# Performance work log

Hardware: AMD Instinct MI355X
Metric: run time of the kernel (lower is better)

## Reference

```python
import jax, jax.numpy as jnp
import numpy as np

N = 16384      # total nodes
E = 262144     # edges (avg degree 16)
HID = 1024     # hidden_dim
D = 768        # internal_dim
R = 6          # num_relations
B = 4          # num_bases
L = 2          # num_gnn_layers
BN_EPS = 1e-5
LN_EPS = 1e-5


def setup_inputs() -> dict:
    key = jax.random.key(0)
    ks = jax.random.split(key, 16)
    s = 0.02
    return {
        "h_text": jax.random.normal(ks[0], (N, HID), jnp.float32),
        "edge_index": jax.random.randint(ks[1], (2, E), 0, N, jnp.int32),
        "edge_type": jax.random.randint(ks[2], (E,), 0, R, jnp.int32),
        # input projection
        "w_in": jax.random.normal(ks[3], (HID, D), jnp.float32) * s,
        "b_in": jnp.zeros((D,), jnp.float32),
        # per-layer RGCN params (stacked over L layers)
        "basis": jax.random.normal(ks[4], (L, B, D, D), jnp.float32) * s,
        "comp": jax.random.normal(ks[5], (L, R, B), jnp.float32),
        "root": jax.random.normal(ks[6], (L, D, D), jnp.float32) * s,
        "conv_bias": jnp.zeros((L, D), jnp.float32),
        # per-layer BatchNorm affine params
        "bn_gamma": jnp.ones((L, D), jnp.float32),
        "bn_beta": jnp.zeros((L, D), jnp.float32),
        # output projection + LayerNorm
        "w_out": jax.random.normal(ks[7], (D, HID), jnp.float32) * s,
        "b_out": jnp.zeros((HID,), jnp.float32),
        "ln_gamma": jnp.ones((HID,), jnp.float32),
        "ln_beta": jnp.zeros((HID,), jnp.float32),
    }


def _rgcn_conv(x, src, dst, edge_type, basis, comp, root, bias):
    """PyG RGCNConv with basis decomposition, per-relation mean aggregation."""
    n = x.shape[0]
    # relation weights: W_r = sum_b comp[r,b] * basis[b]  -> [R, D, D]
    W = jnp.einsum('rb,bio->rio', comp, basis)
    # transform every node by every relation once: [R, N, D]
    h_all = jnp.einsum('ni,rio->rno', x, W)
    # per-(relation, target) in-degree for mean normalization
    counts = jnp.zeros((R, n), x.dtype).at[edge_type, dst].add(1.0)
    norm = 1.0 / counts[edge_type, dst]            # each indexed count >= 1
    msg = h_all[edge_type, src] * norm[:, None]    # [E, D] gathered messages
    agg = jax.ops.segment_sum(msg, dst, num_segments=n)
    return agg + x @ root + bias


def _batchnorm(x, gamma, beta):
    mean = jnp.mean(x, axis=0)
    var = jnp.var(x, axis=0)  # biased, as in torch BN training forward
    return gamma * (x - mean) * jax.lax.rsqrt(var + BN_EPS) + beta


def _layernorm(x, gamma, beta):
    mean = jnp.mean(x, axis=-1, keepdims=True)
    var = jnp.var(x, axis=-1, keepdims=True)
    return gamma * (x - mean) * jax.lax.rsqrt(var + LN_EPS) + beta


def reference(h_text, edge_index, edge_type, w_in, b_in, basis, comp, root,
              conv_bias, bn_gamma, bn_beta, w_out, b_out, ln_gamma, ln_beta):
    src, dst = edge_index[0], edge_index[1]
    x = jax.nn.relu(h_text @ w_in + b_in)
    for l in range(L):
        h_in = x
        x = _rgcn_conv(x, src, dst, edge_type, basis[l], comp[l], root[l], conv_bias[l])
        x = jax.nn.relu(x)
        x = x + h_in
        x = _batchnorm(x, bn_gamma[l], bn_beta[l])
    h_final = x @ w_out + b_out
    return _layernorm(h_final, ln_gamma, ln_beta)
```

## Files before the change

### kernel.cpp

```cpp
#include <hip/hip_runtime.h>
#include <hip/hip_bf16.h>

#define NN 16384
#define NE 262144
#define HIDD 1024
#define DD 768
#define RR 6
#define BB 4
#define LL 2
#define BN_EPS 1e-5f
#define LN_EPS 1e-5f

typedef __attribute__((ext_vector_type(8))) short bf16x8;
typedef __attribute__((ext_vector_type(4))) float f32x4;

__device__ __forceinline__ float b2f(unsigned short u) {
  union { unsigned int i; float f; } c;
  c.i = ((unsigned int)u) << 16;
  return c.f;
}
__device__ __forceinline__ unsigned short f2b(float f) {
  union { float f; unsigned int u; } c;
  c.f = f;
  unsigned int x = c.u;
  x += 0x7FFFu + ((x >> 16) & 1u);
  return (unsigned short)(x >> 16);
}

__device__ __forceinline__ void gll16(const unsigned short* g, unsigned short* l) {
  __builtin_amdgcn_global_load_lds(
      (const __attribute__((address_space(1))) unsigned int*)g,
      (__attribute__((address_space(3))) unsigned int*)l, 16, 0, 0);
}

__global__ void k_detect(const unsigned short* __restrict__ h, int* __restrict__ flag) {
  __shared__ int sh[256];
  int cnt = 0;
  for (int k = 0; k < 256; ++k) {
    ushort4 t = *(const ushort4*)&h[(size_t)(k * 256 + threadIdx.x) * 4];
    if ((t.x & 0x7F80) == 0x7F80) cnt++;
    if ((t.y & 0x7F80) == 0x7F80) cnt++;
    if ((t.z & 0x7F80) == 0x7F80) cnt++;
    if ((t.w & 0x7F80) == 0x7F80) cnt++;
  }
  sh[threadIdx.x] = cnt;
  __syncthreads();
  if (threadIdx.x == 0) {
    int t = 0;
    for (int i = 0; i < 256; ++i) t += sh[i];
    flag[0] = (t > 16) ? 1 : 0;
  }
}

template <int MODE>
__device__ __forceinline__ float load1t(const void* p, size_t i, int isf32) {
  if (MODE == 1 || (MODE == 0 && isf32)) return ((const float*)p)[i];
  return b2f(((const unsigned short*)p)[i]);
}

__global__ void k_cvt8(const void* s0, const void* s1, const void* s2, const void* s3,
                       const void* s4, const void* s5, const void* s6, const void* s7,
                       float* __restrict__ fpar, const int* __restrict__ flagp) {
  const int isf32 = flagp[0];
  const int seg = blockIdx.y;
  const int lens[8] = {768, 48, 1536, 1536, 1536, 1024, 1024, 1024};
  const int offs_[8] = {0, 768, 816, 2352, 3888, 5424, 6448, 7472};
  const void* srcs[8] = {s0, s1, s2, s3, s4, s5, s6, s7};
  int i = blockIdx.x * 256 + threadIdx.x;
  if (i < lens[seg]) fpar[offs_[seg] + i] = load1t<0>(srcs[seg], i, isf32);
}

__global__ void k_cvtb(const void* __restrict__ in, unsigned short* __restrict__ out,
                       int n, const int* __restrict__ flagp) {
  const int isf32 = flagp[0];
  int i = blockIdx.x * 256 + threadIdx.x;
  if (i < n) out[i] = f2b(load1t<0>(in, (size_t)i, isf32));
}

__global__ void k_fill(float* __restrict__ out, long n, float val) {
  long i = (long)blockIdx.x * 256 + threadIdx.x;
  if (i < n) out[i] = val;
}

__global__ __launch_bounds__(256) void k_transpose(const void* __restrict__ src,
                                                   long ioff,
                                                   unsigned short* __restrict__ dst,
                                                   int I, int J, int dstStride,
                                                   int dstOff,
                                                   const int* __restrict__ flagp) {
  const int isf32 = flagp[0];
  __shared__ unsigned short t[64][65];
  const int j0 = blockIdx.x * 64, i0 = blockIdx.y * 64;
  const int tx = threadIdx.x & 63, ty = threadIdx.x >> 6;
  for (int rr = ty; rr < 64; rr += 4)
    t[rr][tx] = f2b(load1t<0>(src, (size_t)ioff + (size_t)(i0 + rr) * J + j0 + tx, isf32));
  __syncthreads();
  for (int rr = ty; rr < 64; rr += 4)
    dst[(size_t)(j0 + rr) * dstStride + dstOff + i0 + tx] = t[tx][rr];
}

__global__ __launch_bounds__(256) void k_tbatch(const void* __restrict__ root, long roff,
                                                const void* __restrict__ basis, long boff,
                                                unsigned short* __restrict__ BT,
                                                const int* __restrict__ flagp) {
  const int isf32 = flagp[0];
  const int z = blockIdx.z;
  const void* src = (z == 0) ? root : basis;
  const long off = (z == 0) ? roff : boff + (long)(z - 1) * DD * DD;
  __shared__ unsigned short t[64][65];
  const int j0 = blockIdx.x * 64, i0 = blockIdx.y * 64;
  const int tx = threadIdx.x & 63, ty = threadIdx.x >> 6;
  for (int rr = ty; rr < 64; rr += 4)
    t[rr][tx] = f2b(load1t<0>(src, (size_t)off + (size_t)(i0 + rr) * DD + j0 + tx, isf32));
  __syncthreads();
  for (int rr = ty; rr < 64; rr += 4)
    BT[(size_t)(j0 + rr) * (5 * DD) + z * DD + i0 + tx] = t[tx][rr];
}

template <int BIAS, int RELU, int OUTB>
__global__ __launch_bounds__(256) void k_mgemm(const unsigned short* __restrict__ A,
                                               const unsigned short* __restrict__ Bt,
                                               const float* __restrict__ bias,
                                               void* __restrict__ C,
                                               int M, int Nn, int K) {
  __shared__ __align__(16) unsigned short Alds[128 * 32];
  __shared__ __align__(16) unsigned short Blds[128 * 32];
  const int tid = threadIdx.x;
  const int lane = tid & 63, w = tid >> 6;
  const int wm = w >> 1, wn = w & 1;
  const int fr = lane & 15, kg = lane >> 4;
  const int nwg = gridDim.x;
  int id = blockIdx.x;
  if ((nwg & 7) == 0) id = (id & 7) * (nwg >> 3) + (id >> 3);
  const int gx = Nn >> 7;
  const int m0 = (id / gx) * 128, n0 = (id % gx) * 128;

  const int srow = w * 16 + (lane >> 2);
  const int sslot = (lane & 3) ^ ((lane >> 3) & 3);
  const unsigned short* ga = A + (size_t)(m0 + srow) * K + sslot * 8;
  const unsigned short* ga2 = ga + (size_t)64 * K;
  const unsigned short* gb = Bt + (size_t)(n0 + srow) * K + sslot * 8;
  const unsigned short* gb2 = gb + (size_t)64 * K;
  unsigned short* la = Alds + w * 512;
  unsigned short* lb = Blds + w * 512;
  const int roff = fr * 32 + ((kg ^ ((fr >> 1) & 3)) * 8);

  f32x4 acc[4][4] = {};

  for (int k0 = 0; k0 < K; k0 += 32) {
    gll16(ga + k0, la);
    gll16(ga2 + k0, la + 2048);
    gll16(gb + k0, lb);
    gll16(gb2 + k0, lb + 2048);
    __syncthreads();
    bf16x8 af[4], bfr[4];
#pragma unroll
    for (int i = 0; i < 4; ++i) {
      af[i] = *(const bf16x8*)(Alds + (wm * 4 + i) * 512 + roff);
      bfr[i] = *(const bf16x8*)(Blds + (wn * 4 + i) * 512 + roff);
    }
#pragma unroll
    for (int i = 0; i < 4; ++i)
#pragma unroll
      for (int j = 0; j < 4; ++j)
        acc[i][j] = __builtin_amdgcn_mfma_f32_16x16x32_bf16(af[i], bfr[j],
                                                            acc[i][j], 0, 0, 0);
    __syncthreads();
  }

  const int orow = (lane >> 4) * 4;
#pragma unroll
  for (int i = 0; i < 4; ++i) {
#pragma unroll
    for (int j = 0; j < 4; ++j) {
      const int n = n0 + wn * 64 + j * 16 + fr;
      const float bv = BIAS ? bias[n] : 0.f;
#pragma unroll
      for (int rg = 0; rg < 4; ++rg) {
        const int m = m0 + wm * 64 + i * 16 + orow + rg;
        const size_t off = (size_t)m * Nn + n;
        float v = acc[i][j][rg] + bv;
        if (RELU) v = fmaxf(v, 0.f);
        if (OUTB) ((unsigned short*)C)[off] = f2b(v);
        else      ((float*)C)[off] = v;
      }
    }
  }
}

__global__ __launch_bounds__(256) void k_mgemm3(const unsigned short* __restrict__ x0,
                                                const unsigned short* __restrict__ Y01,
                                                const unsigned short* __restrict__ Y23,
                                                const unsigned short* __restrict__ BT,
                                                float* __restrict__ C) {
  __shared__ __align__(16) unsigned short Alds[128 * 32];
  __shared__ __align__(16) unsigned short Blds[128 * 32];
  const int tid = threadIdx.x;
  const int lane = tid & 63, w = tid >> 6;
  const int wm = w >> 1, wn = w & 1;
  const int fr = lane & 15, kg = lane >> 4;
  const int nwg = gridDim.x;
  int id = blockIdx.x;
  id = (id & 7) * (nwg >> 3) + (id >> 3);
  const int m0 = (id / 6) * 128, n0 = (id % 6) * 128;

  const int srow = w * 16 + (lane >> 2);
  const int sslot = (lane & 3) ^ ((lane >> 3) & 3);
  const unsigned short* gx = x0 + (size_t)(m0 + srow) * DD + sslot * 8;
  const unsigned short* gx2 = gx + (size_t)64 * DD;
  const unsigned short* gy = Y01 + (size_t)(m0 + srow) * 1536 + sslot * 8;
  const unsigned short* gy2 = gy + (size_t)64 * 1536;
  const unsigned short* gz = Y23 + (size_t)(m0 + srow) * 1536 + sslot * 8;
  const unsigned short* gz2 = gz + (size_t)64 * 1536;
  const unsigned short* gb = BT + (size_t)(n0 + srow) * 3840 + sslot * 8;
  const unsigned short* gb2 = gb + (size_t)64 * 3840;
  unsigned short* la = Alds + w * 512;
  unsigned short* lb = Blds + w * 512;
  const int roff = fr * 32 + ((kg ^ ((fr >> 1) & 3)) * 8);

  f32x4 acc[4][4] = {};

  for (int k0 = 0; k0 < 3840; k0 += 32) {
    const unsigned short *pa, *pa2;
    if (k0 < 768)       { pa = gx + k0;        pa2 = gx2 + k0; }
    else if (k0 < 2304) { pa = gy + k0 - 768;  pa2 = gy2 + k0 - 768; }
    else                { pa = gz + k0 - 2304; pa2 = gz2 + k0 - 2304; }
    gll16(pa, la);
    gll16(pa2, la + 2048);
    gll16(gb + k0, lb);
    gll16(gb2 + k0, lb + 2048);
    __syncthreads();
    bf16x8 af[4], bfr[4];
#pragma unroll
    for (int i = 0; i < 4; ++i) {
      af[i] = *(const bf16x8*)(Alds + (wm * 4 + i) * 512 + roff);
      bfr[i] = *(const bf16x8*)(Blds + (wn * 4 + i) * 512 + roff);
    }
#pragma unroll
    for (int i = 0; i < 4; ++i)
#pragma unroll
      for (int j = 0; j < 4; ++j)
        acc[i][j] = __builtin_amdgcn_mfma_f32_16x16x32_bf16(af[i], bfr[j],
                                                            acc[i][j], 0, 0, 0);
    __syncthreads();
  }

  const int orow = (lane >> 4) * 4;
#pragma unroll
  for (int i = 0; i < 4; ++i) {
#pragma unroll
    for (int j = 0; j < 4; ++j) {
      const int n = n0 + wn * 64 + j * 16 + fr;
#pragma unroll
      for (int rg = 0; rg < 4; ++rg) {
        const int m = m0 + wm * 64 + i * 16 + orow + rg;
        C[(size_t)m * DD + n] = acc[i][j][rg];
      }
    }
  }
}

__global__ void k_count(const int* __restrict__ et, const int* __restrict__ dst,
                        float* __restrict__ counts) {
  int e = blockIdx.x * 256 + threadIdx.x;
  if (e < NE) atomicAdd(&counts[(size_t)et[e] * NN + dst[e]], 1.0f);
}

__global__ void k_deg(const int* __restrict__ dst, int* __restrict__ deg) {
  int e = blockIdx.x * 256 + threadIdx.x;
  if (e < NE) atomicAdd(&deg[dst[e]], 1);
}

__global__ __launch_bounds__(256) void k_scan(const int* __restrict__ deg,
                                              int* __restrict__ offs,
                                              int* __restrict__ cursor) {
  __shared__ int part[256];
  const int base = threadIdx.x * 64;
  int s = 0;
  for (int i = 0; i < 64; ++i) s += deg[base + i];
  part[threadIdx.x] = s;
  __syncthreads();
  if (threadIdx.x == 0) {
    int run = 0;
    for (int i = 0; i < 256; ++i) { int t = part[i]; part[i] = run; run += t; }
  }
  __syncthreads();
  int run = part[threadIdx.x];
  for (int i = 0; i < 64; ++i) {
    offs[base + i] = run;
    cursor[base + i] = run;
    run += deg[base + i];
  }
  if (threadIdx.x == 255) offs[NN] = run;
}

__global__ void k_place(const int* __restrict__ src, const int* __restrict__ dst,
                        const int* __restrict__ et, int* __restrict__ cursor,
                        int* __restrict__ elist) {
  int e = blockIdx.x * 256 + threadIdx.x;
  if (e >= NE) return;
  int d = dst[e];
  int slot = atomicAdd(&cursor[d], 1);
  elist[slot] = src[e] | (et[e] << 20);
}

__global__ __launch_bounds__(192) void k_gather4(const int* __restrict__ offs,
                                                 const int* __restrict__ elist,
                                                 const float* __restrict__ counts,
                                                 const float* __restrict__ compL,
                                                 const unsigned short* __restrict__ x0,
                                                 unsigned short* __restrict__ Y01,
                                                 unsigned short* __restrict__ Y23) {
  const int d = blockIdx.x;
  const int tid = threadIdx.x;
  __shared__ float sw[RR][4];
  if (tid < 4 * RR) {
    const int r = tid >> 2, j = tid & 3;
    const float c = counts[(size_t)r * NN + d];
    sw[r][j] = (c > 0.f) ? compL[r * BB + j] / c : 0.f;
  }
  __syncthreads();
  const int beg = offs[d], end = offs[d + 1];
  float a0[4] = {}, a1[4] = {}, a2[4] = {}, a3[4] = {};
  int e = beg;
  for (; e + 1 < end; e += 2) {
    const int v1 = elist[e], v2 = elist[e + 1];
    const int s1 = v1 & 0xFFFFF, r1 = v1 >> 20;
    const int s2 = v2 & 0xFFFFF, r2 = v2 >> 20;
    ushort4 t1 = *(const ushort4*)&x0[(size_t)s1 * DD + tid * 4];
    ushort4 t2 = *(const ushort4*)&x0[(size_t)s2 * DD + tid * 4];
    const float f1[4] = {b2f(t1.x), b2f(t1.y), b2f(t1.z), b2f(t1.w)};
    const float f2[4] = {b2f(t2.x), b2f(t2.y), b2f(t2.z), b2f(t2.w)};
#pragma unroll
    for (int c = 0; c < 4; ++c) {
      a0[c] += sw[r1][0] * f1[c] + sw[r2][0] * f2[c];
      a1[c] += sw[r1][1] * f1[c] + sw[r2][1] * f2[c];
      a2[c] += sw[r1][2] * f1[c] + sw[r2][2] * f2[c];
      a3[c] += sw[r1][3] * f1[c] + sw[r2][3] * f2[c];
    }
  }
  if (e < end) {
    const int v = elist[e];
    const int s = v & 0xFFFFF, r = v >> 20;
    ushort4 t = *(const ushort4*)&x0[(size_t)s * DD + tid * 4];
    const float f[4] = {b2f(t.x), b2f(t.y), b2f(t.z), b2f(t.w)};
#pragma unroll
    for (int c = 0; c < 4; ++c) {
      a0[c] += sw[r][0] * f[c];
      a1[c] += sw[r][1] * f[c];
      a2[c] += sw[r][2] * f[c];
      a3[c] += sw[r][3] * f[c];
    }
  }
  ushort4 o;
  o.x = f2b(a0[0]); o.y = f2b(a0[1]); o.z = f2b(a0[2]); o.w = f2b(a0[3]);
  *(ushort4*)&Y01[(size_t)d * 1536 + tid * 4] = o;
  o.x = f2b(a1[0]); o.y = f2b(a1[1]); o.z = f2b(a1[2]); o.w = f2b(a1[3]);
  *(ushort4*)&Y01[(size_t)d * 1536 + DD + tid * 4] = o;
  o.x = f2b(a2[0]); o.y = f2b(a2[1]); o.z = f2b(a2[2]); o.w = f2b(a2[3]);
  *(ushort4*)&Y23[(size_t)d * 1536 + tid * 4] = o;
  o.x = f2b(a3[0]); o.y = f2b(a3[1]); o.z = f2b(a3[2]); o.w = f2b(a3[3]);
  *(ushort4*)&Y23[(size_t)d * 1536 + DD + tid * 4] = o;
}

__global__ __launch_bounds__(256) void k_epi_stats(const float* __restrict__ xc,
                                                   const unsigned short* __restrict__ x0,
                                                   const float* __restrict__ cbias,
                                                   unsigned short* __restrict__ yb,
                                                   float* __restrict__ sums,
                                                   float* __restrict__ sqs) {
  const int r0 = blockIdx.x * 64;
  float lsum[3] = {0.f, 0.f, 0.f}, lsq[3] = {0.f, 0.f, 0.f};
  float cb[3];
#pragma unroll
  for (int j = 0; j < 3; ++j) cb[j] = cbias[threadIdx.x + j * 256];
  for (int i = 0; i < 64; ++i) {
    const size_t row = r0 + i;
#pragma unroll
    for (int j = 0; j < 3; ++j) {
      const int c = threadIdx.x + j * 256;
      float v = xc[row * DD + c];
      v = fmaxf(v + cb[j], 0.f) + b2f(x0[row * DD + c]);
      yb[row * DD + c] = f2b(v);
      lsum[j] += v;
      lsq[j] += v * v;
    }
  }
#pragma unroll
  for (int j = 0; j < 3; ++j) {
    atomicAdd(&sums[threadIdx.x + j * 256], lsum[j]);
    atomicAdd(&sqs[threadIdx.x + j * 256], lsq[j]);
  }
}

__global__ void k_bn_apply(const unsigned short* __restrict__ yb,
                           const float* __restrict__ gamma,
                           const float* __restrict__ beta,
                           const float* __restrict__ sums,
                           const float* __restrict__ sqs,
                           unsigned short* __restrict__ xout) {
  size_t idx = (size_t)blockIdx.x * 256 + threadIdx.x;
  if (idx >= (size_t)NN * DD) return;
  int c = idx % DD;
  float mu = sums[c] * (1.0f / NN);
  float var = sqs[c] * (1.0f / NN) - mu * mu;
  xout[idx] = f2b(gamma[c] * (b2f(yb[idx]) - mu) * rsqrtf(var + BN_EPS) + beta[c]);
}

__global__ __launch_bounds__(256) void k_layernorm(const float* __restrict__ hf,
                                                   const float* __restrict__ gamma,
                                                   const float* __restrict__ beta,
                                                   float* __restrict__ out) {
  const int row = blockIdx.x;
  const float* h = hf + (size_t)row * HIDD;
  float v[4];
  float s = 0.f, sq = 0.f;
#pragma unroll
  for (int j = 0; j < 4; ++j) {
    v[j] = h[threadIdx.x + j * 256];
    s += v[j];
    sq += v[j] * v[j];
  }
#pragma unroll
  for (int off = 32; off > 0; off >>= 1) {
    s += __shfl_down(s, off);
    sq += __shfl_down(sq, off);
  }
  __shared__ float ps[4], pq[4];
  const int lane = threadIdx.x & 63, wv = threadIdx.x >> 6;
  if (lane == 0) { ps[wv] = s; pq[wv] = sq; }
  __syncthreads();
  if (threadIdx.x == 0) {
    float ts = ps[0] + ps[1] + ps[2] + ps[3];
    float tq = pq[0] + pq[1] + pq[2] + pq[3];
    float mu = ts * (1.0f / HIDD);
    float var = tq * (1.0f / HIDD) - mu * mu;
    ps[0] = mu;
    pq[0] = rsqrtf(var + LN_EPS);
  }
  __syncthreads();
  const float mu = ps[0], rstd = pq[0];
#pragma unroll
  for (int j = 0; j < 4; ++j) {
    const int c = threadIdx.x + j * 256;
    out[(size_t)row * HIDD + c] = gamma[c] * (v[j] - mu) * rstd + beta[c];
  }
}

extern "C" void kernel_launch(void* const* d_in, const int* in_sizes, int n_in,
                              void* d_out, int out_size, void* d_ws, size_t ws_size,
                              hipStream_t stream) {
  const void* h_text = d_in[0];
  const int* ei      = (const int*)d_in[1];
  const int* etype   = (const int*)d_in[2];
  const void* w_in  = d_in[3];
  const void* b_in  = d_in[4];
  const void* basis = d_in[5];
  const void* comp  = d_in[6];
  const void* root  = d_in[7];
  const void* convb = d_in[8];
  const void* bn_g  = d_in[9];
  const void* bn_b  = d_in[10];
  const void* w_out = d_in[11];
  const void* b_out = d_in[12];
  const void* ln_g  = d_in[13];
  const void* ln_b  = d_in[14];
  float* out = (float*)d_out;

  const int* src = ei;
  const int* dst = ei + NE;

  char* W = (char*)d_ws;
  int*   flags  = (int*)(W + 0);
  float* stats  = (float*)(W + 256);
  float* fpar   = (float*)(W + 6400);
  float* f_bin  = fpar;
  float* f_comp = fpar + 768;
  float* f_cb   = fpar + 816;
  float* f_bng  = fpar + 2352;
  float* f_bnb  = fpar + 3888;
  float* f_bout = fpar + 5424;
  float* f_lng  = fpar + 6448;
  float* f_lnb  = fpar + 7472;
  float* counts = (float*)(W + 40384);
  int*   deg    = (int*)(W + 433600);
  int*   offs   = (int*)(W + 499136);
  int*   cursor = (int*)(W + 564736);
  int*   elist  = (int*)(W + 630272);
  unsigned short* BTcat = (unsigned short*)(W + 1678848);
  unsigned short* x0    = (unsigned short*)(W + 7577088);
  unsigned short* Y23   = (unsigned short*)(W + 32742912);
  float*          xc    = (float*)(W + 83074560);
  const size_t NEED_B = 133406208;
  if (ws_size < NEED_B) {
    k_fill<<<(int)(((long)out_size + 255) / 256), 256, 0, stream>>>(
        out, (long)out_size, (float)(ws_size >> 20) * 100.0f);
    return;
  }

  unsigned short* h16   = (unsigned short*)d_out;
  unsigned short* wt_in = (unsigned short*)d_out + 29360128;
  unsigned short* Y01   = (unsigned short*)d_out;
  unsigned short* yb    = (unsigned short*)d_out;
  float* hf = out;
  unsigned short* wt_out = BTcat;

  k_detect<<<1, 256, 0, stream>>>((const unsigned short*)h_text, flags);
  {
    dim3 g(6, 8);
    k_cvt8<<<g, 256, 0, stream>>>(b_in, comp, convb, bn_g, bn_b, b_out, ln_g,
                                  ln_b, fpar, flags);
  }

  k_cvtb<<<(NN * HIDD) / 256, 256, 0, stream>>>(h_text, h16, NN * HIDD, flags);
  {
    dim3 g(DD / 64, HIDD / 64);
    k_transpose<<<g, 256, 0, stream>>>(w_in, 0, wt_in, HIDD, DD, HIDD, 0, flags);
  }

  k_mgemm<1, 1, 1><<<(DD / 128) * (NN / 128), 256, 0, stream>>>(
      h16, wt_in, f_bin, x0, NN, DD, HIDD);

  hipMemsetAsync(counts, 0, (size_t)RR * NN * sizeof(float), stream);
  k_count<<<NE / 256, 256, 0, stream>>>(etype, dst, counts);
  hipMemsetAsync(deg, 0, NN * sizeof(int), stream);
  k_deg<<<NE / 256, 256, 0, stream>>>(dst, deg);
  k_scan<<<1, 256, 0, stream>>>(deg, offs, cursor);
  k_place<<<NE / 256, 256, 0, stream>>>(src, dst, etype, cursor, elist);

  for (int l = 0; l < LL; ++l) {
    const long boff = (long)l * BB * DD * DD;
    const long roff = (long)l * DD * DD;
    const float* compL = f_comp + l * RR * BB;
    const float* cbL   = f_cb + l * DD;
    const float* gL    = f_bng + l * DD;
    const float* bL    = f_bnb + l * DD;

    k_gather4<<<NN, 192, 0, stream>>>(offs, elist, counts, compL, x0, Y01, Y23);
    {
      dim3 g(DD / 64, DD / 64, 5);
      k_tbatch<<<g, 256, 0, stream>>>(root, roff, basis, boff, BTcat, flags);
    }
    k_mgemm3<<<(DD / 128) * (NN / 128), 256, 0, stream>>>(x0, Y01, Y23, BTcat, xc);

    hipMemsetAsync(stats, 0, 2 * DD * sizeof(float), stream);
    k_epi_stats<<<NN / 64, 256, 0, stream>>>(xc, x0, cbL, yb, stats, stats + DD);
    k_bn_apply<<<(int)(((size_t)NN * DD + 255) / 256), 256, 0, stream>>>(
        yb, gL, bL, stats, stats + DD, x0);
  }

  {
    dim3 g(HIDD / 64, DD / 64);
    k_transpose<<<g, 256, 0, stream>>>(w_out, 0, wt_out, DD, HIDD, DD, 0, flags);
  }
  k_mgemm<1, 0, 0><<<(HIDD / 128) * (NN / 128), 256, 0, stream>>>(
      x0, wt_out, f_bout, hf, NN, HIDD, DD);

  k_layernorm<<<NN, 256, 0, stream>>>(hf, f_lng, f_lnb, out);
}
```

Baseline: 881.0 us.

## Double-buffer LDS tiles in GEMM kernels and unroll edge gather by four

```diff
diff --git a/kernel.cpp b/kernel.cpp
--- a/kernel.cpp
+++ b/kernel.cpp
@@ -123,8 +123,8 @@
                                                const float* __restrict__ bias,
                                                void* __restrict__ C,
                                                int M, int Nn, int K) {
-  __shared__ __align__(16) unsigned short Alds[128 * 32];
-  __shared__ __align__(16) unsigned short Blds[128 * 32];
+  __shared__ __align__(16) unsigned short Alds[2][128 * 32];
+  __shared__ __align__(16) unsigned short Blds[2][128 * 32];
   const int tid = threadIdx.x;
   const int lane = tid & 63, w = tid >> 6;
   const int wm = w >> 1, wn = w & 1;
@@ -141,23 +141,31 @@
   const unsigned short* ga2 = ga + (size_t)64 * K;
   const unsigned short* gb = Bt + (size_t)(n0 + srow) * K + sslot * 8;
   const unsigned short* gb2 = gb + (size_t)64 * K;
-  unsigned short* la = Alds + w * 512;
-  unsigned short* lb = Blds + w * 512;
+  const int wo = w * 512;
   const int roff = fr * 32 + ((kg ^ ((fr >> 1) & 3)) * 8);
 
   f32x4 acc[4][4] = {};
 
+  gll16(ga, &Alds[0][wo]);
+  gll16(ga2, &Alds[0][wo + 2048]);
+  gll16(gb, &Blds[0][wo]);
+  gll16(gb2, &Blds[0][wo + 2048]);
+  __syncthreads();
+
   for (int k0 = 0; k0 < K; k0 += 32) {
-    gll16(ga + k0, la);
-    gll16(ga2 + k0, la + 2048);
-    gll16(gb + k0, lb);
-    gll16(gb2 + k0, lb + 2048);
-    __syncthreads();
+    const int cur = (k0 >> 5) & 1;
+    const int nxt = cur ^ 1;
+    if (k0 + 32 < K) {
+      gll16(ga + k0 + 32, &Alds[nxt][wo]);
+      gll16(ga2 + k0 + 32, &Alds[nxt][wo + 2048]);
+      gll16(gb + k0 + 32, &Blds[nxt][wo]);
+      gll16(gb2 + k0 + 32, &Blds[nxt][wo + 2048]);
+    }
     bf16x8 af[4], bfr[4];
 #pragma unroll
     for (int i = 0; i < 4; ++i) {
-      af[i] = *(const bf16x8*)(Alds + (wm * 4 + i) * 512 + roff);
-      bfr[i] = *(const bf16x8*)(Blds + (wn * 4 + i) * 512 + roff);
+      af[i] = *(const bf16x8*)(&Alds[cur][(wm * 4 + i) * 512 + roff]);
+      bfr[i] = *(const bf16x8*)(&Blds[cur][(wn * 4 + i) * 512 + roff]);
     }
 #pragma unroll
     for (int i = 0; i < 4; ++i)
@@ -193,8 +201,8 @@
                                                 const unsigned short* __restrict__ Y23,
                                                 const unsigned short* __restrict__ BT,
                                                 float* __restrict__ C) {
-  __shared__ __align__(16) unsigned short Alds[128 * 32];
-  __shared__ __align__(16) unsigned short Blds[128 * 32];
+  __shared__ __align__(16) unsigned short Alds[2][128 * 32];
+  __shared__ __align__(16) unsigned short Blds[2][128 * 32];
   const int tid = threadIdx.x;
   const int lane = tid & 63, w = tid >> 6;
   const int wm = w >> 1, wn = w & 1;
@@ -206,35 +214,41 @@
 
   const int srow = w * 16 + (lane >> 2);
   const int sslot = (lane & 3) ^ ((lane >> 3) & 3);
-  const unsigned short* gx = x0 + (size_t)(m0 + srow) * DD + sslot * 8;
-  const unsigned short* gx2 = gx + (size_t)64 * DD;
+  const unsigned short* gxp = x0 + (size_t)(m0 + srow) * DD + sslot * 8;
+  const unsigned short* gxp2 = gxp + (size_t)64 * DD;
   const unsigned short* gy = Y01 + (size_t)(m0 + srow) * 1536 + sslot * 8;
   const unsigned short* gy2 = gy + (size_t)64 * 1536;
   const unsigned short* gz = Y23 + (size_t)(m0 + srow) * 1536 + sslot * 8;
   const unsigned short* gz2 = gz + (size_t)64 * 1536;
   const unsigned short* gb = BT + (size_t)(n0 + srow) * 3840 + sslot * 8;
   const unsigned short* gb2 = gb + (size_t)64 * 3840;
-  unsigned short* la = Alds + w * 512;
-  unsigned short* lb = Blds + w * 512;
+  const int wo = w * 512;
   const int roff = fr * 32 + ((kg ^ ((fr >> 1) & 3)) * 8);
 
   f32x4 acc[4][4] = {};
 
-  for (int k0 = 0; k0 < 3840; k0 += 32) {
+  auto stage = [&](int k0, int b) {
     const unsigned short *pa, *pa2;
-    if (k0 < 768)       { pa = gx + k0;        pa2 = gx2 + k0; }
+    if (k0 < 768)       { pa = gxp + k0;       pa2 = gxp2 + k0; }
     else if (k0 < 2304) { pa = gy + k0 - 768;  pa2 = gy2 + k0 - 768; }
     else                { pa = gz + k0 - 2304; pa2 = gz2 + k0 - 2304; }
-    gll16(pa, la);
-    gll16(pa2, la + 2048);
-    gll16(gb + k0, lb);
-    gll16(gb2 + k0, lb + 2048);
-    __syncthreads();
+    gll16(pa, &Alds[b][wo]);
+    gll16(pa2, &Alds[b][wo + 2048]);
+    gll16(gb + k0, &Blds[b][wo]);
+    gll16(gb2 + k0, &Blds[b][wo + 2048]);
+  };
+
+  stage(0, 0);
+  __syncthreads();
+
+  for (int k0 = 0; k0 < 3840; k0 += 32) {
+    const int cur = (k0 >> 5) & 1;
+    if (k0 + 32 < 3840) stage(k0 + 32, cur ^ 1);
     bf16x8 af[4], bfr[4];
 #pragma unroll
     for (int i = 0; i < 4; ++i) {
-      af[i] = *(const bf16x8*)(Alds + (wm * 4 + i) * 512 + roff);
-      bfr[i] = *(const bf16x8*)(Blds + (wn * 4 + i) * 512 + roff);
+      af[i] = *(const bf16x8*)(&Alds[cur][(wm * 4 + i) * 512 + roff]);
+      bfr[i] = *(const bf16x8*)(&Blds[cur][(wn * 4 + i) * 512 + roff]);
     }
 #pragma unroll
     for (int i = 0; i < 4; ++i)
@@ -323,23 +337,29 @@
   const int beg = offs[d], end = offs[d + 1];
   float a0[4] = {}, a1[4] = {}, a2[4] = {}, a3[4] = {};
   int e = beg;
-  for (; e + 1 < end; e += 2) {
-    const int v1 = elist[e], v2 = elist[e + 1];
+  for (; e + 3 < end; e += 4) {
+    const int v1 = elist[e], v2 = elist[e + 1], v3 = elist[e + 2], v4 = elist[e + 3];
     const int s1 = v1 & 0xFFFFF, r1 = v1 >> 20;
     const int s2 = v2 & 0xFFFFF, r2 = v2 >> 20;
+    const int s3 = v3 & 0xFFFFF, r3 = v3 >> 20;
+    const int s4 = v4 & 0xFFFFF, r4 = v4 >> 20;
     ushort4 t1 = *(const ushort4*)&x0[(size_t)s1 * DD + tid * 4];
     ushort4 t2 = *(const ushort4*)&x0[(size_t)s2 * DD + tid * 4];
+    ushort4 t3 = *(const ushort4*)&x0[(size_t)s3 * DD + tid * 4];
+    ushort4 t4 = *(const ushort4*)&x0[(size_t)s4 * DD + tid * 4];
     const float f1[4] = {b2f(t1.x), b2f(t1.y), b2f(t1.z), b2f(t1.w)};
     const float f2[4] = {b2f(t2.x), b2f(t2.y), b2f(t2.z), b2f(t2.w)};
+    const float f3[4] = {b2f(t3.x), b2f(t3.y), b2f(t3.z), b2f(t3.w)};
+    const float f4[4] = {b2f(t4.x), b2f(t4.y), b2f(t4.z), b2f(t4.w)};
 #pragma unroll
     for (int c = 0; c < 4; ++c) {
-      a0[c] += sw[r1][0] * f1[c] + sw[r2][0] * f2[c];
-      a1[c] += sw[r1][1] * f1[c] + sw[r2][1] * f2[c];
-      a2[c] += sw[r1][2] * f1[c] + sw[r2][2] * f2[c];
-      a3[c] += sw[r1][3] * f1[c] + sw[r2][3] * f2[c];
-    }
-  }
-  if (e < end) {
+      a0[c] += sw[r1][0] * f1[c] + sw[r2][0] * f2[c] + sw[r3][0] * f3[c] + sw[r4][0] * f4[c];
+      a1[c] += sw[r1][1] * f1[c] + sw[r2][1] * f2[c] + sw[r3][1] * f3[c] + sw[r4][1] * f4[c];
+      a2[c] += sw[r1][2] * f1[c] + sw[r2][2] * f2[c] + sw[r3][2] * f3[c] + sw[r4][2] * f4[c];
+      a3[c] += sw[r1][3] * f1[c] + sw[r2][3] * f2[c] + sw[r3][3] * f3[c] + sw[r4][3] * f4[c];
+    }
+  }
+  for (; e < end; ++e) {
     const int v = elist[e];
     const int s = v & 0xFFFFF, r = v >> 20;
     ushort4 t = *(const ushort4*)&x0[(size_t)s * DD + tid * 4];
```

After: 923.5 us. 4.8% more time.
